# Performance work log

Measured on AMD Instinct MI355X. Metric: run time of the kernel, lower is better.

Reference implementation:

```python
import jax, jax.numpy as jnp
import numpy as np

K, R, A, F, T = 100000, 5, 8, 32, 96
ROTATION_DELTA = 1


def setup_inputs() -> dict:
    key = jax.random.key(0)
    k1, k2, k3, k4, k5, k6, k7 = jax.random.split(key, 7)
    # barycentric coordinates: last dim packs (vertex_index, weight)
    idx = jax.random.randint(k1, (K, R, A, 3), 0, K)
    w = jax.random.uniform(k2, (K, R, A, 3), dtype=jnp.float32)
    w = w / jnp.sum(w, axis=-1, keepdims=True)
    bary_coordinates = jnp.stack([idx.astype(jnp.float32), w], axis=-1)  # (K,R,A,3,2)
    mesh_signal = jax.random.normal(k3, (K, F), dtype=jnp.float32)
    # kernel from define_kernel_values (abstract): fixed prior interpolation weights (R,A,R,A)
    kernel = jax.random.normal(k4, (R, A, R, A), dtype=jnp.float32) * 0.1
    template_neighbor_weights = jax.random.normal(k5, (T, R, A, F), dtype=jnp.float32) * 0.05
    template_self_weights = jax.random.normal(k6, (T, 1, F), dtype=jnp.float32) * 0.05
    bias = jax.random.normal(k7, (T,), dtype=jnp.float32) * 0.01
    return {
        "mesh_signal": mesh_signal,
        "bary_coordinates": bary_coordinates,
        "kernel": kernel,
        "template_neighbor_weights": template_neighbor_weights,
        "template_self_weights": template_self_weights,
        "bias": bias,
    }


def reference(mesh_signal, bary_coordinates, kernel, template_neighbor_weights,
              template_self_weights, bias):
    # --- signal retrieval: barycentric gather + interpolation ---
    idx = bary_coordinates[..., 0].astype(jnp.int32)          # (K,R,A,3)
    bw = bary_coordinates[..., 1]                              # (K,R,A,3)
    gathered = mesh_signal[idx]                                # (K,R,A,3,F)
    interp = jnp.sum(bw[..., None] * gathered, axis=-2)        # (K,R,A,F)
    # --- prior kernel fold (include_prior=True) ---
    interp = jnp.einsum('raxy,kxyf->kraf', kernel, interp)     # (K,R,A,F)
    # --- center contribution ---
    conv_center = jnp.einsum('tef,kf->ket', template_self_weights, mesh_signal)  # (K,1,T)
    # --- per-rotation template fold (torch.range is end-inclusive -> A//delta + 1 rotations) ---
    orientations = list(range(0, A + 1, ROTATION_DELTA))
    conv_neighbor = jnp.stack(
        [jnp.einsum('traf,kraf->kt', template_neighbor_weights,
                    jnp.roll(interp, o, axis=2)) + bias
         for o in orientations],
        axis=1)                                                # (K,O,T)
    return jax.nn.relu(conv_center + conv_neighbor)            # (K,O,T)
```

## Files before the change

kernel.cpp:

```cpp
#include <hip/hip_runtime.h>
#include <hip/hip_bf16.h>
#include <stdint.h>


typedef __attribute__((ext_vector_type(8))) short short8;
typedef __attribute__((ext_vector_type(4))) float floatx4;
typedef __attribute__((ext_vector_type(2))) float fx2;

#define KPTS 100000
#define OUT_STRIDE 864
#define BM 64
#define THREADS 512
#define BP_SHORTS 1007616

#define BARRIER() do {                              \
    __builtin_amdgcn_sched_barrier(0);              \
    asm volatile("s_waitcnt lgkmcnt(0)");           \
    __builtin_amdgcn_s_barrier();                   \
  } while (0)

__device__ __forceinline__ short f2bf(float x) {
  union { float f; uint32_t u; } c; c.f = x;
  uint32_t u = c.u;
  u += 0x7FFFu + ((u >> 16) & 1u);
  return (short)(u >> 16);
}
__device__ __forceinline__ float bf2f(short s) {
  union { uint32_t u; float f; } c;
  c.u = ((uint32_t)(uint16_t)s) << 16;
  return c.f;
}

__global__ void prep_ms(const float* __restrict__ ms, short* __restrict__ msb) {
  const int i = (blockIdx.x * 256 + threadIdx.x) * 8;
  if (i < KPTS * 32) {
    floatx4 a = *(const floatx4*)(ms + i);
    floatx4 b = *(const floatx4*)(ms + i + 4);
    short8 s;
#pragma unroll
    for (int j = 0; j < 4; ++j) { s[j] = f2bf(a[j]); s[4 + j] = f2bf(b[j]); }
    *reinterpret_cast<short8*>(msb + i) = s;
  }
}

__global__ void prep_B(const float* __restrict__ kern,
                       const float* __restrict__ tw,
                       const float* __restrict__ sw,
                       short* __restrict__ Bp) {
  const int ntile = blockIdx.x;
  const int ch    = blockIdx.y;
  const int lane  = threadIdx.x;
  const int n = ntile * 16 + (lane & 15);
  const int o = n / 96;
  const int t = n - o * 96;
  const int fb = (lane >> 4) * 8;

  short8 v;
  if (ch < 40) {
    float kcol[40];
#pragma unroll
    for (int ra = 0; ra < 40; ++ra) kcol[ra] = kern[ra * 40 + ch];
#pragma unroll
    for (int j = 0; j < 8; ++j) {
      const int f = fb + j;
      float acc = 0.f;
      for (int r = 0; r < 5; ++r) {
#pragma unroll
        for (int a = 0; a < 8; ++a) {
          acc += kcol[r * 8 + a] * tw[((t * 5 + r) * 8 + ((a + o) & 7)) * 32 + f];
        }
      }
      v[j] = f2bf(acc);
    }
  } else {
#pragma unroll
    for (int j = 0; j < 8; ++j) v[j] = f2bf(sw[t * 32 + fb + j]);
  }
  *reinterpret_cast<short8*>(Bp + ((size_t)(ch * 48 + ntile) * 64 + lane) * 8) = v;
}

__global__ __launch_bounds__(THREADS, 1) void conv_main(
    const short* __restrict__ msb,
    const float* __restrict__ bary,
    const float* __restrict__ bias,
    const short* __restrict__ Bp,
    float* __restrict__ out) {
  __shared__ short Atile[2][BM][40];

  const int kbase = blockIdx.x * BM;
  const int tid = threadIdx.x;
  const int lane = tid & 63;
  const int wn = tid >> 6;
  const int l15 = lane & 15;
  const int kh = lane >> 4;

  const bool builder = tid < 256;
  const int arow = tid >> 2;
  const int af0 = (tid & 3) * 8;
  const int krow = kbase + (arow & 63);
  const bool rowok = builder && (krow < KPTS);
  const float* __restrict__ brow = bary + (size_t)(rowok ? krow : 0) * 240;
  const short* __restrict__ mrowb = msb + (size_t)(rowok ? krow : 0) * 32 + af0;

  fx2 bE0, bE1, bE2, bO0, bO1, bO2;
  short8 eG0, eG1, eG2, oG0, oG1, oG2;
  float eW0, eW1, eW2, oW0, oW1, oW2;

  auto ldbary = [&](int c, fx2& p0, fx2& p1, fx2& p2) {
    if (rowok) {
      const fx2* bp = (const fx2*)(brow + c * 6);
      p0 = __builtin_nontemporal_load(bp);
      p1 = __builtin_nontemporal_load(bp + 1);
      p2 = __builtin_nontemporal_load(bp + 2);
    } else {
      p0 = (fx2)0.f; p1 = (fx2)0.f; p2 = (fx2)0.f;
    }
  };
  auto issueG = [&](int c, const fx2& p0, const fx2& p1, const fx2& p2,
                    short8& A, short8& B, short8& C,
                    float& W0, float& W1, float& W2) {
    if (c == 40) {
      A = *(const short8*)(mrowb);
      B = A; C = A;
      W0 = rowok ? 1.f : 0.f; W1 = 0.f; W2 = 0.f;
    } else {
      A = *(const short8*)(msb + ((size_t)(int)p0.x) * 32 + af0);
      B = *(const short8*)(msb + ((size_t)(int)p1.x) * 32 + af0);
      C = *(const short8*)(msb + ((size_t)(int)p2.x) * 32 + af0);
      W0 = p0.y; W1 = p1.y; W2 = p2.y;
    }
  };
  auto commitG = [&](const short8& A, const short8& B, const short8& C,
                     float W0, float W1, float W2, int buf) {
    short8 s;
#pragma unroll
    for (int j = 0; j < 8; ++j)
      s[j] = f2bf(W0 * bf2f(A[j]) + W1 * bf2f(B[j]) + W2 * bf2f(C[j]));
    *reinterpret_cast<short8*>(&Atile[buf][arow][af0]) = s;
  };

  short8 bfA[6], bfB[6];
  auto loadB = [&](int c, short8* dst) {
    const short* bp = Bp + ((size_t)(c * 48 + wn * 6) * 64 + lane) * 8;
#pragma unroll
    for (int j = 0; j < 6; ++j)
      dst[j] = *reinterpret_cast<const short8*>(bp + (size_t)j * 512);
  };

  floatx4 acc[4][6];
#pragma unroll
  for (int mi = 0; mi < 4; ++mi)
#pragma unroll
    for (int nj = 0; nj < 6; ++nj) acc[mi][nj] = (floatx4)0.f;

  if (builder) {
    fx2 t0, t1, t2;
    ldbary(0, t0, t1, t2);
    issueG(0, t0, t1, t2, eG0, eG1, eG2, eW0, eW1, eW2);
    ldbary(1, t0, t1, t2);
    issueG(1, t0, t1, t2, oG0, oG1, oG2, oW0, oW1, oW2);
    ldbary(2, bE0, bE1, bE2);
    commitG(eG0, eG1, eG2, eW0, eW1, eW2, 0);
  }
  loadB(0, bfA);
  BARRIER();

#define ITER(ch, UB0, UB1, UB2, FB0, FB1, FB2,                                  \
             FG0, FG1, FG2, FW0, FW1, FW2,                                      \
             CG0, CG1, CG2, CW0, CW1, CW2, CUR, BF, NBF)                        \
  {                                                                             \
    if (builder) {                                                              \
      if ((ch) + 2 <= 40)                                                       \
        issueG((ch) + 2, UB0, UB1, UB2, FG0, FG1, FG2, FW0, FW1, FW2);          \
      if ((ch) + 3 <= 39) ldbary((ch) + 3, FB0, FB1, FB2);                      \
    }                                                                           \
    short8 af[4];                                                               \
    _Pragma("unroll")                                                           \
    for (int mi = 0; mi < 4; ++mi)                                              \
      af[mi] = *reinterpret_cast<const short8*>(&Atile[CUR][mi * 16 + l15][kh * 8]); \
    if ((ch) + 1 <= 40) loadB((ch) + 1, NBF);                                   \
    _Pragma("unroll")                                                           \
    for (int nj = 0; nj < 6; ++nj)                                              \
      _Pragma("unroll")                                                         \
      for (int mi = 0; mi < 4; ++mi)                                            \
        acc[mi][nj] = __builtin_amdgcn_mfma_f32_16x16x32_bf16(af[mi], BF[nj],   \
                                                              acc[mi][nj], 0, 0, 0); \
    if (builder && (ch) + 1 <= 40)                                              \
      commitG(CG0, CG1, CG2, CW0, CW1, CW2, (CUR) ^ 1);                         \
    BARRIER();                                                                  \
  }

  for (int ch = 0; ch < 40; ch += 2) {
    ITER(ch,     bE0, bE1, bE2, bO0, bO1, bO2,
         eG0, eG1, eG2, eW0, eW1, eW2,
         oG0, oG1, oG2, oW0, oW1, oW2, 0, bfA, bfB)
    ITER(ch + 1, bO0, bO1, bO2, bE0, bE1, bE2,
         oG0, oG1, oG2, oW0, oW1, oW2,
         eG0, eG1, eG2, eW0, eW1, eW2, 1, bfB, bfA)
  }
  ITER(40, bE0, bE1, bE2, bO0, bO1, bO2,
       eG0, eG1, eG2, eW0, eW1, eW2,
       oG0, oG1, oG2, oW0, oW1, oW2, 0, bfA, bfB)
#undef ITER

#pragma unroll
  for (int mi = 0; mi < 4; ++mi) {
    const int rb = kbase + mi * 16 + kh * 4;
#pragma unroll
    for (int nj = 0; nj < 6; ++nj) {
      const int n = wn * 96 + nj * 16 + l15;
      const float bsv = bias[nj * 16 + l15];
      const bool dup = (wn == 0);
#pragma unroll
      for (int i = 0; i < 4; ++i) {
        const int r = rb + i;
        if (r < KPTS) {
          float vv = fmaxf(acc[mi][nj][i] + bsv, 0.f);
          out[(size_t)r * OUT_STRIDE + n] = vv;
          if (dup) out[(size_t)r * OUT_STRIDE + 768 + n] = vv;
        }
      }
    }
  }
}

extern "C" void kernel_launch(void* const* d_in, const int* in_sizes, int n_in,
                              void* d_out, int out_size, void* d_ws, size_t ws_size,
                              hipStream_t stream) {
  const float* ms   = (const float*)d_in[0];
  const float* bary = (const float*)d_in[1];
  const float* kern = (const float*)d_in[2];
  const float* tw   = (const float*)d_in[3];
  const float* sw   = (const float*)d_in[4];
  const float* bias = (const float*)d_in[5];
  float* out = (float*)d_out;
  short* Bp  = (short*)d_ws;
  short* msb = (short*)d_ws + BP_SHORTS;

  hipLaunchKernelGGL(prep_B, dim3(48, 41), dim3(64), 0, stream, kern, tw, sw, Bp);
  hipLaunchKernelGGL(prep_ms, dim3((KPTS * 32 / 8 + 255) / 256), dim3(256), 0, stream,
                     ms, msb);
  hipLaunchKernelGGL(conv_main, dim3(1563), dim3(THREADS), 0, stream,
                     msb, bary, bias, Bp, out);
}
```

Baseline: 483.2 us.

## Process two K-chunks per barrier interval with a double-width A tile

Widens the LDS A tile so that each barrier interval builds and consumes two 32-wide K-chunks instead of one. This halves the number of block-wide barriers across the 41-chunk reduction. The barycentric prefetch distance is lengthened, and B-fragment loads are interleaved between the two MFMA halves. The cost is more live registers for gathered rows and prefetched bary values, plus a larger LDS tile.

```diff
diff --git a/kernel.cpp b/kernel.cpp
--- a/kernel.cpp
+++ b/kernel.cpp
@@ -85,7 +85,7 @@
     const float* __restrict__ bias,
     const short* __restrict__ Bp,
     float* __restrict__ out) {
-  __shared__ short Atile[2][BM][40];
+  __shared__ short Atile[2][BM][68];
 
   const int kbase = blockIdx.x * BM;
   const int tid = threadIdx.x;
@@ -102,9 +102,10 @@
   const float* __restrict__ brow = bary + (size_t)(rowok ? krow : 0) * 240;
   const short* __restrict__ mrowb = msb + (size_t)(rowok ? krow : 0) * 32 + af0;
 
-  fx2 bE0, bE1, bE2, bO0, bO1, bO2;
-  short8 eG0, eG1, eG2, oG0, oG1, oG2;
-  float eW0, eW1, eW2, oW0, oW1, oW2;
+  fx2 bEa0, bEa1, bEa2, bEb0, bEb1, bEb2;
+  fx2 bOa0, bOa1, bOa2, bOb0, bOb1, bOb2;
+  short8 G0, G1, G2, G3, G4, G5;
+  float W0, W1, W2, W3, W4, W5;
 
   auto ldbary = [&](int c, fx2& p0, fx2& p1, fx2& p2) {
     if (rowok) {
@@ -118,25 +119,25 @@
   };
   auto issueG = [&](int c, const fx2& p0, const fx2& p1, const fx2& p2,
                     short8& A, short8& B, short8& C,
-                    float& W0, float& W1, float& W2) {
+                    float& V0, float& V1, float& V2) {
     if (c == 40) {
       A = *(const short8*)(mrowb);
       B = A; C = A;
-      W0 = rowok ? 1.f : 0.f; W1 = 0.f; W2 = 0.f;
+      V0 = rowok ? 1.f : 0.f; V1 = 0.f; V2 = 0.f;
     } else {
       A = *(const short8*)(msb + ((size_t)(int)p0.x) * 32 + af0);
       B = *(const short8*)(msb + ((size_t)(int)p1.x) * 32 + af0);
       C = *(const short8*)(msb + ((size_t)(int)p2.x) * 32 + af0);
-      W0 = p0.y; W1 = p1.y; W2 = p2.y;
+      V0 = p0.y; V1 = p1.y; V2 = p2.y;
     }
   };
   auto commitG = [&](const short8& A, const short8& B, const short8& C,
-                     float W0, float W1, float W2, int buf) {
+                     float V0, float V1, float V2, int buf, int half) {
     short8 s;
 #pragma unroll
     for (int j = 0; j < 8; ++j)
-      s[j] = f2bf(W0 * bf2f(A[j]) + W1 * bf2f(B[j]) + W2 * bf2f(C[j]));
-    *reinterpret_cast<short8*>(&Atile[buf][arow][af0]) = s;
+      s[j] = f2bf(V0 * bf2f(A[j]) + V1 * bf2f(B[j]) + V2 * bf2f(C[j]));
+    *reinterpret_cast<short8*>(&Atile[buf][arow][half * 32 + af0]) = s;
   };
 
   short8 bfA[6], bfB[6];
@@ -156,52 +157,78 @@
   if (builder) {
     fx2 t0, t1, t2;
     ldbary(0, t0, t1, t2);
-    issueG(0, t0, t1, t2, eG0, eG1, eG2, eW0, eW1, eW2);
+    issueG(0, t0, t1, t2, G0, G1, G2, W0, W1, W2);
     ldbary(1, t0, t1, t2);
-    issueG(1, t0, t1, t2, oG0, oG1, oG2, oW0, oW1, oW2);
-    ldbary(2, bE0, bE1, bE2);
-    commitG(eG0, eG1, eG2, eW0, eW1, eW2, 0);
+    issueG(1, t0, t1, t2, G3, G4, G5, W3, W4, W5);
+    ldbary(2, bEa0, bEa1, bEa2);
+    ldbary(3, bEb0, bEb1, bEb2);
+    ldbary(4, bOa0, bOa1, bOa2);
+    ldbary(5, bOb0, bOb1, bOb2);
+    commitG(G0, G1, G2, W0, W1, W2, 0, 0);
+    commitG(G3, G4, G5, W3, W4, W5, 0, 1);
   }
   loadB(0, bfA);
   BARRIER();
 
-#define ITER(ch, UB0, UB1, UB2, FB0, FB1, FB2,                                  \
-             FG0, FG1, FG2, FW0, FW1, FW2,                                      \
-             CG0, CG1, CG2, CW0, CW1, CW2, CUR, BF, NBF)                        \
+#define INTERVAL(i, QA0, QA1, QA2, QB0, QB1, QB2)                               \
   {                                                                             \
+    const int cur = (i) & 1;                                                    \
+    loadB(2 * (i) + 1, bfB);                                                    \
     if (builder) {                                                              \
-      if ((ch) + 2 <= 40)                                                       \
-        issueG((ch) + 2, UB0, UB1, UB2, FG0, FG1, FG2, FW0, FW1, FW2);          \
-      if ((ch) + 3 <= 39) ldbary((ch) + 3, FB0, FB1, FB2);                      \
+      if (2 * (i) + 2 <= 40)                                                    \
+        issueG(2 * (i) + 2, QA0, QA1, QA2, G0, G1, G2, W0, W1, W2);             \
+      if (2 * (i) + 3 <= 39)                                                    \
+        issueG(2 * (i) + 3, QB0, QB1, QB2, G3, G4, G5, W3, W4, W5);             \
+      if (2 * (i) + 6 <= 39) ldbary(2 * (i) + 6, QA0, QA1, QA2);                \
+      if (2 * (i) + 7 <= 39) ldbary(2 * (i) + 7, QB0, QB1, QB2);                \
     }                                                                           \
     short8 af[4];                                                               \
     _Pragma("unroll")                                                           \
     for (int mi = 0; mi < 4; ++mi)                                              \
-      af[mi] = *reinterpret_cast<const short8*>(&Atile[CUR][mi * 16 + l15][kh * 8]); \
-    if ((ch) + 1 <= 40) loadB((ch) + 1, NBF);                                   \
+      af[mi] = *reinterpret_cast<const short8*>(&Atile[cur][mi * 16 + l15][kh * 8]); \
     _Pragma("unroll")                                                           \
     for (int nj = 0; nj < 6; ++nj)                                              \
       _Pragma("unroll")                                                         \
       for (int mi = 0; mi < 4; ++mi)                                            \
-        acc[mi][nj] = __builtin_amdgcn_mfma_f32_16x16x32_bf16(af[mi], BF[nj],   \
+        acc[mi][nj] = __builtin_amdgcn_mfma_f32_16x16x32_bf16(af[mi], bfA[nj],  \
                                                               acc[mi][nj], 0, 0, 0); \
-    if (builder && (ch) + 1 <= 40)                                              \
-      commitG(CG0, CG1, CG2, CW0, CW1, CW2, (CUR) ^ 1);                         \
+    if (2 * (i) + 2 <= 40) loadB(2 * (i) + 2, bfA);                             \
+    _Pragma("unroll")                                                           \
+    for (int mi = 0; mi < 4; ++mi)                                              \
+      af[mi] = *reinterpret_cast<const short8*>(&Atile[cur][mi * 16 + l15][32 + kh * 8]); \
+    _Pragma("unroll")                                                           \
+    for (int nj = 0; nj < 6; ++nj)                                              \
+      _Pragma("unroll")                                                         \
+      for (int mi = 0; mi < 4; ++mi)                                            \
+        acc[mi][nj] = __builtin_amdgcn_mfma_f32_16x16x32_bf16(af[mi], bfB[nj],  \
+                                                              acc[mi][nj], 0, 0, 0); \
+    if (builder) {                                                              \
+      if (2 * (i) + 2 <= 40)                                                    \
+        commitG(G0, G1, G2, W0, W1, W2, cur ^ 1, 0);                            \
+      if (2 * (i) + 3 <= 39)                                                    \
+        commitG(G3, G4, G5, W3, W4, W5, cur ^ 1, 1);                            \
+    }                                                                           \
     BARRIER();                                                                  \
   }
 
-  for (int ch = 0; ch < 40; ch += 2) {
-    ITER(ch,     bE0, bE1, bE2, bO0, bO1, bO2,
-         eG0, eG1, eG2, eW0, eW1, eW2,
-         oG0, oG1, oG2, oW0, oW1, oW2, 0, bfA, bfB)
-    ITER(ch + 1, bO0, bO1, bO2, bE0, bE1, bE2,
-         oG0, oG1, oG2, oW0, oW1, oW2,
-         eG0, eG1, eG2, eW0, eW1, eW2, 1, bfB, bfA)
-  }
-  ITER(40, bE0, bE1, bE2, bO0, bO1, bO2,
-       eG0, eG1, eG2, eW0, eW1, eW2,
-       oG0, oG1, oG2, oW0, oW1, oW2, 0, bfA, bfB)
-#undef ITER
+  for (int ii = 0; ii < 20; ii += 2) {
+    INTERVAL(ii,     bEa0, bEa1, bEa2, bEb0, bEb1, bEb2)
+    INTERVAL(ii + 1, bOa0, bOa1, bOa2, bOb0, bOb1, bOb2)
+  }
+#undef INTERVAL
+
+  {
+    short8 af[4];
+#pragma unroll
+    for (int mi = 0; mi < 4; ++mi)
+      af[mi] = *reinterpret_cast<const short8*>(&Atile[0][mi * 16 + l15][kh * 8]);
+#pragma unroll
+    for (int nj = 0; nj < 6; ++nj)
+#pragma unroll
+      for (int mi = 0; mi < 4; ++mi)
+        acc[mi][nj] = __builtin_amdgcn_mfma_f32_16x16x32_bf16(af[mi], bfA[nj],
+                                                              acc[mi][nj], 0, 0, 0);
+  }
 
 #pragma unroll
   for (int mi = 0; mi < 4; ++mi) {
```

Result: slower. 512.4 us (+6.1%).

## Split fused gather-interpolate GEMM into separate interpolation and GEMM kernels

Applied to the files above, without the earlier changes.

The barycentric gather and interpolation move out of the GEMM kernel into a standalone high-occupancy kernel, `interp_A`. It writes the bf16 A operand per row into the unused space of the output buffer. The GEMM kernel then streams A and B straight from global memory into registers with simple register double-buffering, with no LDS tile and no block barriers. The aim is to hide random-gather latency with many waves instead of half the threads of a single-occupancy block. The cost is an extra global write and read of the intermediate, plus reliance on each block reading its own output rows before overwriting them.

```diff
diff --git a/kernel.cpp b/kernel.cpp
--- a/kernel.cpp
+++ b/kernel.cpp
@@ -9,15 +9,9 @@
 
 #define KPTS 100000
 #define OUT_STRIDE 864
-#define BM 64
+#define ROW_BYTES 3456
 #define THREADS 512
 #define BP_SHORTS 1007616
-
-#define BARRIER() do {                              \
-    __builtin_amdgcn_sched_barrier(0);              \
-    asm volatile("s_waitcnt lgkmcnt(0)");           \
-    __builtin_amdgcn_s_barrier();                   \
-  } while (0)
 
 __device__ __forceinline__ short f2bf(float x) {
   union { float f; uint32_t u; } c; c.f = x;
@@ -79,67 +73,61 @@
   *reinterpret_cast<short8*>(Bp + ((size_t)(ch * 48 + ntile) * 64 + lane) * 8) = v;
 }
 
-__global__ __launch_bounds__(THREADS, 1) void conv_main(
+__global__ __launch_bounds__(256, 8) void interp_A(
     const short* __restrict__ msb,
     const float* __restrict__ bary,
+    char* __restrict__ apb) {
+  const int w = blockIdx.x * 4 + (threadIdx.x >> 6);
+  if (w >= 6250 * 41) return;
+  const int lane = threadIdx.x & 63;
+  const int ktile = w / 41;
+  const int ch = w - ktile * 41;
+  const int row = ktile * 16 + (lane & 15);
+  const int fb = (lane >> 4) * 8;
+
+  short8 v;
+  if (ch == 40) {
+    v = *(const short8*)(msb + (size_t)row * 32 + fb);
+  } else {
+    const float* bp = bary + (size_t)row * 240 + ch * 6;
+    fx2 p0 = __builtin_nontemporal_load((const fx2*)bp);
+    fx2 p1 = __builtin_nontemporal_load((const fx2*)(bp + 2));
+    fx2 p2 = __builtin_nontemporal_load((const fx2*)(bp + 4));
+    short8 A = *(const short8*)(msb + ((size_t)(int)p0.x) * 32 + fb);
+    short8 B = *(const short8*)(msb + ((size_t)(int)p1.x) * 32 + fb);
+    short8 C = *(const short8*)(msb + ((size_t)(int)p2.x) * 32 + fb);
+#pragma unroll
+    for (int j = 0; j < 8; ++j)
+      v[j] = f2bf(p0.y * bf2f(A[j]) + p1.y * bf2f(B[j]) + p2.y * bf2f(C[j]));
+  }
+  *reinterpret_cast<short8*>(apb + (size_t)row * ROW_BYTES + ch * 64 + (lane >> 4) * 16) = v;
+}
+
+__global__ __launch_bounds__(THREADS, 1) void gemm_main(
+    const char* __restrict__ apb,
+    const short* __restrict__ Bp,
     const float* __restrict__ bias,
-    const short* __restrict__ Bp,
     float* __restrict__ out) {
-  __shared__ short Atile[2][BM][40];
-
-  const int kbase = blockIdx.x * BM;
+  const int kbase = blockIdx.x * 64;
   const int tid = threadIdx.x;
   const int lane = tid & 63;
   const int wn = tid >> 6;
   const int l15 = lane & 15;
   const int kh = lane >> 4;
 
-  const bool builder = tid < 256;
-  const int arow = tid >> 2;
-  const int af0 = (tid & 3) * 8;
-  const int krow = kbase + (arow & 63);
-  const bool rowok = builder && (krow < KPTS);
-  const float* __restrict__ brow = bary + (size_t)(rowok ? krow : 0) * 240;
-  const short* __restrict__ mrowb = msb + (size_t)(rowok ? krow : 0) * 32 + af0;
-
-  fx2 bE0, bE1, bE2, bO0, bO1, bO2;
-  short8 eG0, eG1, eG2, oG0, oG1, oG2;
-  float eW0, eW1, eW2, oW0, oW1, oW2;
-
-  auto ldbary = [&](int c, fx2& p0, fx2& p1, fx2& p2) {
-    if (rowok) {
-      const fx2* bp = (const fx2*)(brow + c * 6);
-      p0 = __builtin_nontemporal_load(bp);
-      p1 = __builtin_nontemporal_load(bp + 1);
-      p2 = __builtin_nontemporal_load(bp + 2);
-    } else {
-      p0 = (fx2)0.f; p1 = (fx2)0.f; p2 = (fx2)0.f;
-    }
+  int rowm[4];
+#pragma unroll
+  for (int mi = 0; mi < 4; ++mi) {
+    int r = kbase + mi * 16 + l15;
+    rowm[mi] = (r < KPTS) ? r : (KPTS - 1);
+  }
+
+  auto loadA = [&](int c, short8* dst) {
+#pragma unroll
+    for (int mi = 0; mi < 4; ++mi)
+      dst[mi] = *reinterpret_cast<const short8*>(
+          apb + (size_t)rowm[mi] * ROW_BYTES + c * 64 + kh * 16);
   };
-  auto issueG = [&](int c, const fx2& p0, const fx2& p1, const fx2& p2,
-                    short8& A, short8& B, short8& C,
-                    float& W0, float& W1, float& W2) {
-    if (c == 40) {
-      A = *(const short8*)(mrowb);
-      B = A; C = A;
-      W0 = rowok ? 1.f : 0.f; W1 = 0.f; W2 = 0.f;
-    } else {
-      A = *(const short8*)(msb + ((size_t)(int)p0.x) * 32 + af0);
-      B = *(const short8*)(msb + ((size_t)(int)p1.x) * 32 + af0);
-      C = *(const short8*)(msb + ((size_t)(int)p2.x) * 32 + af0);
-      W0 = p0.y; W1 = p1.y; W2 = p2.y;
-    }
-  };
-  auto commitG = [&](const short8& A, const short8& B, const short8& C,
-                     float W0, float W1, float W2, int buf) {
-    short8 s;
-#pragma unroll
-    for (int j = 0; j < 8; ++j)
-      s[j] = f2bf(W0 * bf2f(A[j]) + W1 * bf2f(B[j]) + W2 * bf2f(C[j]));
-    *reinterpret_cast<short8*>(&Atile[buf][arow][af0]) = s;
-  };
-
-  short8 bfA[6], bfB[6];
   auto loadB = [&](int c, short8* dst) {
     const short* bp = Bp + ((size_t)(c * 48 + wn * 6) * 64 + lane) * 8;
 #pragma unroll
@@ -153,55 +141,23 @@
 #pragma unroll
     for (int nj = 0; nj < 6; ++nj) acc[mi][nj] = (floatx4)0.f;
 
-  if (builder) {
-    fx2 t0, t1, t2;
-    ldbary(0, t0, t1, t2);
-    issueG(0, t0, t1, t2, eG0, eG1, eG2, eW0, eW1, eW2);
-    ldbary(1, t0, t1, t2);
-    issueG(1, t0, t1, t2, oG0, oG1, oG2, oW0, oW1, oW2);
-    ldbary(2, bE0, bE1, bE2);
-    commitG(eG0, eG1, eG2, eW0, eW1, eW2, 0);
-  }
-  loadB(0, bfA);
-  BARRIER();
-
-#define ITER(ch, UB0, UB1, UB2, FB0, FB1, FB2,                                  \
-             FG0, FG1, FG2, FW0, FW1, FW2,                                      \
-             CG0, CG1, CG2, CW0, CW1, CW2, CUR, BF, NBF)                        \
-  {                                                                             \
-    if (builder) {                                                              \
-      if ((ch) + 2 <= 40)                                                       \
-        issueG((ch) + 2, UB0, UB1, UB2, FG0, FG1, FG2, FW0, FW1, FW2);          \
-      if ((ch) + 3 <= 39) ldbary((ch) + 3, FB0, FB1, FB2);                      \
-    }                                                                           \
-    short8 af[4];                                                               \
-    _Pragma("unroll")                                                           \
-    for (int mi = 0; mi < 4; ++mi)                                              \
-      af[mi] = *reinterpret_cast<const short8*>(&Atile[CUR][mi * 16 + l15][kh * 8]); \
-    if ((ch) + 1 <= 40) loadB((ch) + 1, NBF);                                   \
-    _Pragma("unroll")                                                           \
-    for (int nj = 0; nj < 6; ++nj)                                              \
-      _Pragma("unroll")                                                         \
-      for (int mi = 0; mi < 4; ++mi)                                            \
-        acc[mi][nj] = __builtin_amdgcn_mfma_f32_16x16x32_bf16(af[mi], BF[nj],   \
-                                                              acc[mi][nj], 0, 0, 0); \
-    if (builder && (ch) + 1 <= 40)                                              \
-      commitG(CG0, CG1, CG2, CW0, CW1, CW2, (CUR) ^ 1);                         \
-    BARRIER();                                                                  \
-  }
-
-  for (int ch = 0; ch < 40; ch += 2) {
-    ITER(ch,     bE0, bE1, bE2, bO0, bO1, bO2,
-         eG0, eG1, eG2, eW0, eW1, eW2,
-         oG0, oG1, oG2, oW0, oW1, oW2, 0, bfA, bfB)
-    ITER(ch + 1, bO0, bO1, bO2, bE0, bE1, bE2,
-         oG0, oG1, oG2, oW0, oW1, oW2,
-         eG0, eG1, eG2, eW0, eW1, eW2, 1, bfB, bfA)
-  }
-  ITER(40, bE0, bE1, bE2, bO0, bO1, bO2,
-       eG0, eG1, eG2, eW0, eW1, eW2,
-       oG0, oG1, oG2, oW0, oW1, oW2, 0, bfA, bfB)
-#undef ITER
+  short8 af[4], bf[6], naf[4], nbf[6];
+  loadA(0, af);
+  loadB(0, bf);
+
+  for (int ch = 0; ch < 41; ++ch) {
+    if (ch < 40) { loadA(ch + 1, naf); loadB(ch + 1, nbf); }
+#pragma unroll
+    for (int nj = 0; nj < 6; ++nj)
+#pragma unroll
+      for (int mi = 0; mi < 4; ++mi)
+        acc[mi][nj] = __builtin_amdgcn_mfma_f32_16x16x32_bf16(af[mi], bf[nj],
+                                                              acc[mi][nj], 0, 0, 0);
+#pragma unroll
+    for (int mi = 0; mi < 4; ++mi) af[mi] = naf[mi];
+#pragma unroll
+    for (int nj = 0; nj < 6; ++nj) bf[nj] = nbf[nj];
+  }
 
 #pragma unroll
   for (int mi = 0; mi < 4; ++mi) {
@@ -236,10 +192,13 @@
   float* out = (float*)d_out;
   short* Bp  = (short*)d_ws;
   short* msb = (short*)d_ws + BP_SHORTS;
+  char* apb  = (char*)d_out;
 
   hipLaunchKernelGGL(prep_B, dim3(48, 41), dim3(64), 0, stream, kern, tw, sw, Bp);
   hipLaunchKernelGGL(prep_ms, dim3((KPTS * 32 / 8 + 255) / 256), dim3(256), 0, stream,
                      ms, msb);
-  hipLaunchKernelGGL(conv_main, dim3(1563), dim3(THREADS), 0, stream,
-                     msb, bary, bias, Bp, out);
-}
+  hipLaunchKernelGGL(interp_A, dim3((6250 * 41 + 3) / 4), dim3(256), 0, stream,
+                     msb, bary, apb);
+  hipLaunchKernelGGL(gemm_main, dim3(1563), dim3(THREADS), 0, stream,
+                     apb, Bp, bias, out);
+}
```

After: 785.4 us. 1.63x slower.

## Split N across 16 waves per block and simplify gather pipeline to single-stage

Applied to the files above, without the earlier changes.

The main conv kernel now launches 1024 threads (16 waves) per block, each wave covering 3 N-tiles instead of 6, which halves the per-wave accumulator and B-fragment register footprint. The launch bound asks for 4 blocks per CU, aiming to raise occupancy for hiding gather latency. The two-deep register-staged gather/bary prefetch pipeline and the B-fragment double buffer are removed in favour of a simpler one-chunk-ahead scheme, with B loaded in the same iteration it is used. This trades explicit software prefetching for more waves to hide latency, and B load latency is now exposed inside each iteration.

```diff
diff --git a/kernel.cpp b/kernel.cpp
--- a/kernel.cpp
+++ b/kernel.cpp
@@ -10,7 +10,6 @@
 #define KPTS 100000
 #define OUT_STRIDE 864
 #define BM 64
-#define THREADS 512
 #define BP_SHORTS 1007616
 
 #define BARRIER() do {                              \
@@ -79,7 +78,7 @@
   *reinterpret_cast<short8*>(Bp + ((size_t)(ch * 48 + ntile) * 64 + lane) * 8) = v;
 }
 
-__global__ __launch_bounds__(THREADS, 1) void conv_main(
+__global__ __launch_bounds__(1024, 4) void conv_main(
     const short* __restrict__ msb,
     const float* __restrict__ bary,
     const float* __restrict__ bias,
@@ -90,7 +89,7 @@
   const int kbase = blockIdx.x * BM;
   const int tid = threadIdx.x;
   const int lane = tid & 63;
-  const int wn = tid >> 6;
+  const int wid = tid >> 6;
   const int l15 = lane & 15;
   const int kh = lane >> 4;
 
@@ -102,115 +101,93 @@
   const float* __restrict__ brow = bary + (size_t)(rowok ? krow : 0) * 240;
   const short* __restrict__ mrowb = msb + (size_t)(rowok ? krow : 0) * 32 + af0;
 
-  fx2 bE0, bE1, bE2, bO0, bO1, bO2;
-  short8 eG0, eG1, eG2, oG0, oG1, oG2;
-  float eW0, eW1, eW2, oW0, oW1, oW2;
-
-  auto ldbary = [&](int c, fx2& p0, fx2& p1, fx2& p2) {
+  fx2 q0, q1, q2;
+  short8 G0, G1, G2;
+  float W0, W1, W2;
+
+  auto ldbary = [&](int c) {
     if (rowok) {
       const fx2* bp = (const fx2*)(brow + c * 6);
-      p0 = __builtin_nontemporal_load(bp);
-      p1 = __builtin_nontemporal_load(bp + 1);
-      p2 = __builtin_nontemporal_load(bp + 2);
+      q0 = __builtin_nontemporal_load(bp);
+      q1 = __builtin_nontemporal_load(bp + 1);
+      q2 = __builtin_nontemporal_load(bp + 2);
     } else {
-      p0 = (fx2)0.f; p1 = (fx2)0.f; p2 = (fx2)0.f;
-    }
-  };
-  auto issueG = [&](int c, const fx2& p0, const fx2& p1, const fx2& p2,
-                    short8& A, short8& B, short8& C,
-                    float& W0, float& W1, float& W2) {
+      q0 = (fx2)0.f; q1 = (fx2)0.f; q2 = (fx2)0.f;
+    }
+  };
+  auto issueG = [&](int c) {
     if (c == 40) {
-      A = *(const short8*)(mrowb);
-      B = A; C = A;
+      G0 = *(const short8*)(mrowb);
+      G1 = G0; G2 = G0;
       W0 = rowok ? 1.f : 0.f; W1 = 0.f; W2 = 0.f;
     } else {
-      A = *(const short8*)(msb + ((size_t)(int)p0.x) * 32 + af0);
-      B = *(const short8*)(msb + ((size_t)(int)p1.x) * 32 + af0);
-      C = *(const short8*)(msb + ((size_t)(int)p2.x) * 32 + af0);
-      W0 = p0.y; W1 = p1.y; W2 = p2.y;
-    }
-  };
-  auto commitG = [&](const short8& A, const short8& B, const short8& C,
-                     float W0, float W1, float W2, int buf) {
+      G0 = *(const short8*)(msb + ((size_t)(int)q0.x) * 32 + af0);
+      G1 = *(const short8*)(msb + ((size_t)(int)q1.x) * 32 + af0);
+      G2 = *(const short8*)(msb + ((size_t)(int)q2.x) * 32 + af0);
+      W0 = q0.y; W1 = q1.y; W2 = q2.y;
+    }
+  };
+  auto commitG = [&](int buf) {
     short8 s;
 #pragma unroll
     for (int j = 0; j < 8; ++j)
-      s[j] = f2bf(W0 * bf2f(A[j]) + W1 * bf2f(B[j]) + W2 * bf2f(C[j]));
+      s[j] = f2bf(W0 * bf2f(G0[j]) + W1 * bf2f(G1[j]) + W2 * bf2f(G2[j]));
     *reinterpret_cast<short8*>(&Atile[buf][arow][af0]) = s;
   };
 
-  short8 bfA[6], bfB[6];
-  auto loadB = [&](int c, short8* dst) {
-    const short* bp = Bp + ((size_t)(c * 48 + wn * 6) * 64 + lane) * 8;
-#pragma unroll
-    for (int j = 0; j < 6; ++j)
-      dst[j] = *reinterpret_cast<const short8*>(bp + (size_t)j * 512);
-  };
-
-  floatx4 acc[4][6];
+  short8 bf[3];
+  auto loadB = [&](int c) {
+    const short* bp = Bp + ((size_t)(c * 48 + wid * 3) * 64 + lane) * 8;
+#pragma unroll
+    for (int j = 0; j < 3; ++j)
+      bf[j] = *reinterpret_cast<const short8*>(bp + (size_t)j * 512);
+  };
+
+  floatx4 acc[4][3];
 #pragma unroll
   for (int mi = 0; mi < 4; ++mi)
 #pragma unroll
-    for (int nj = 0; nj < 6; ++nj) acc[mi][nj] = (floatx4)0.f;
+    for (int nj = 0; nj < 3; ++nj) acc[mi][nj] = (floatx4)0.f;
 
   if (builder) {
-    fx2 t0, t1, t2;
-    ldbary(0, t0, t1, t2);
-    issueG(0, t0, t1, t2, eG0, eG1, eG2, eW0, eW1, eW2);
-    ldbary(1, t0, t1, t2);
-    issueG(1, t0, t1, t2, oG0, oG1, oG2, oW0, oW1, oW2);
-    ldbary(2, bE0, bE1, bE2);
-    commitG(eG0, eG1, eG2, eW0, eW1, eW2, 0);
-  }
-  loadB(0, bfA);
+    ldbary(0);
+    issueG(0);
+    commitG(0);
+    ldbary(1);
+  }
   BARRIER();
 
-#define ITER(ch, UB0, UB1, UB2, FB0, FB1, FB2,                                  \
-             FG0, FG1, FG2, FW0, FW1, FW2,                                      \
-             CG0, CG1, CG2, CW0, CW1, CW2, CUR, BF, NBF)                        \
-  {                                                                             \
-    if (builder) {                                                              \
-      if ((ch) + 2 <= 40)                                                       \
-        issueG((ch) + 2, UB0, UB1, UB2, FG0, FG1, FG2, FW0, FW1, FW2);          \
-      if ((ch) + 3 <= 39) ldbary((ch) + 3, FB0, FB1, FB2);                      \
-    }                                                                           \
-    short8 af[4];                                                               \
-    _Pragma("unroll")                                                           \
-    for (int mi = 0; mi < 4; ++mi)                                              \
-      af[mi] = *reinterpret_cast<const short8*>(&Atile[CUR][mi * 16 + l15][kh * 8]); \
-    if ((ch) + 1 <= 40) loadB((ch) + 1, NBF);                                   \
-    _Pragma("unroll")                                                           \
-    for (int nj = 0; nj < 6; ++nj)                                              \
-      _Pragma("unroll")                                                         \
-      for (int mi = 0; mi < 4; ++mi)                                            \
-        acc[mi][nj] = __builtin_amdgcn_mfma_f32_16x16x32_bf16(af[mi], BF[nj],   \
-                                                              acc[mi][nj], 0, 0, 0); \
-    if (builder && (ch) + 1 <= 40)                                              \
-      commitG(CG0, CG1, CG2, CW0, CW1, CW2, (CUR) ^ 1);                         \
-    BARRIER();                                                                  \
-  }
-
-  for (int ch = 0; ch < 40; ch += 2) {
-    ITER(ch,     bE0, bE1, bE2, bO0, bO1, bO2,
-         eG0, eG1, eG2, eW0, eW1, eW2,
-         oG0, oG1, oG2, oW0, oW1, oW2, 0, bfA, bfB)
-    ITER(ch + 1, bO0, bO1, bO2, bE0, bE1, bE2,
-         oG0, oG1, oG2, oW0, oW1, oW2,
-         eG0, eG1, eG2, eW0, eW1, eW2, 1, bfB, bfA)
-  }
-  ITER(40, bE0, bE1, bE2, bO0, bO1, bO2,
-       eG0, eG1, eG2, eW0, eW1, eW2,
-       oG0, oG1, oG2, oW0, oW1, oW2, 0, bfA, bfB)
-#undef ITER
+  for (int ch = 0; ch <= 40; ++ch) {
+    const int cur = ch & 1;
+    if (builder) {
+      if (ch < 40) issueG(ch + 1);
+      if (ch + 2 <= 39) ldbary(ch + 2);
+    }
+    loadB(ch);
+
+    short8 af[4];
+#pragma unroll
+    for (int mi = 0; mi < 4; ++mi)
+      af[mi] = *reinterpret_cast<const short8*>(&Atile[cur][mi * 16 + l15][kh * 8]);
+#pragma unroll
+    for (int nj = 0; nj < 3; ++nj)
+#pragma unroll
+      for (int mi = 0; mi < 4; ++mi)
+        acc[mi][nj] = __builtin_amdgcn_mfma_f32_16x16x32_bf16(af[mi], bf[nj],
+                                                              acc[mi][nj], 0, 0, 0);
+
+    if (builder && ch < 40) commitG(cur ^ 1);
+    BARRIER();
+  }
 
 #pragma unroll
   for (int mi = 0; mi < 4; ++mi) {
     const int rb = kbase + mi * 16 + kh * 4;
 #pragma unroll
-    for (int nj = 0; nj < 6; ++nj) {
-      const int n = wn * 96 + nj * 16 + l15;
-      const float bsv = bias[nj * 16 + l15];
-      const bool dup = (wn == 0);
+    for (int nj = 0; nj < 3; ++nj) {
+      const int n = wid * 48 + nj * 16 + l15;
+      const float bsv = bias[(wid & 1) * 48 + nj * 16 + l15];
+      const bool dup = (n < 96);
 #pragma unroll
       for (int i = 0; i < 4; ++i) {
         const int r = rb + i;
@@ -240,6 +217,6 @@
   hipLaunchKernelGGL(prep_B, dim3(48, 41), dim3(64), 0, stream, kern, tw, sw, Bp);
   hipLaunchKernelGGL(prep_ms, dim3((KPTS * 32 / 8 + 255) / 256), dim3(256), 0, stream,
                      ms, msb);
-  hipLaunchKernelGGL(conv_main, dim3(1563), dim3(THREADS), 0, stream,
+  hipLaunchKernelGGL(conv_main, dim3(1563), dim3(1024), 0, stream,
                      msb, bary, bias, Bp, out);
 }
```

Measured after the change: 598.2 us. 1.24x slower.
